# Optimization experiments

Measured on AMD Instinct MI355X. Metric: run time of the kernel, lower is better.

The kernel has to match this reference:

```python
import jax, jax.numpy as jnp
import numpy as np

EPS = 1e-6

def setup_inputs() -> dict:
    key = jax.random.key(0)
    ks = jax.random.split(key, 9)
    B, H, M = 8192, 1024, 16
    Hh = H // 2
    s = lambda k, shape, fan: jax.random.normal(k, shape, jnp.float32) * (1.0 / np.sqrt(fan))
    return {
        "query_embedding": jax.random.normal(ks[0], (B, H), jnp.float32),
        "cls1_w": s(ks[1], (Hh, H), H),
        "cls1_b": jnp.zeros((Hh,), jnp.float32),
        "cls3_w": s(ks[2], (M, Hh), Hh),
        "cls3_b": jnp.zeros((M,), jnp.float32),
        "exp_w1": s(ks[3], (M, Hh, H), H),
        "exp_b1": jnp.zeros((M, Hh), jnp.float32),
        "exp_w2": s(ks[4], (M, H, Hh), Hh),
        "exp_b2": jnp.zeros((M, H), jnp.float32),
    }

def _l2_normalize(x, eps=EPS):
    # F.normalize: x / clamp(||x||_2, min=eps)
    n = jnp.sqrt(jnp.sum(x * x, axis=-1, keepdims=True))
    return x / jnp.maximum(n, eps)

def reference(query_embedding, cls1_w, cls1_b, cls3_w, cls3_b,
              exp_w1, exp_b1, exp_w2, exp_b2):
    q = query_embedding  # [B, H]
    # --- cls(): gating network (eval, sbmoe_top1) ---
    x1 = jax.nn.relu(q @ cls1_w.T + cls1_b)          # [B, H/2]
    logits = x1 @ cls3_w.T + cls3_b                  # [B, M]
    probs = jax.nn.softmax(logits, axis=-1)          # [B, M]
    top1 = jnp.argmax(probs, axis=-1)                # [B]
    mask = jax.nn.one_hot(top1, probs.shape[-1], dtype=probs.dtype)
    gates = probs * mask                             # [B, M] (one nonzero/row)
    # --- query_embedder(): run all experts, gate, combine ---
    h = jax.nn.relu(jnp.einsum('bd,mhd->bmh', q, exp_w1) + exp_b1)   # [B, M, H/2]
    expert_out = jnp.einsum('bmh,mdh->bmd', h, exp_w2) + exp_b2      # [B, M, H]
    combined = jnp.einsum('bmd,bm->bd', expert_out, gates)           # [B, H]
    out = _l2_normalize(combined) + q
    return out
```

## Files before the change

### kernel.cpp

```cpp
#include <hip/hip_runtime.h>
#include <math.h>

#define NB 8192
#define H 1024
#define HH 512
#define NEXP 16
#define NT128 96
#define AMBIG_THR 1e-3f

typedef __attribute__((ext_vector_type(8))) short bfrag;
typedef __attribute__((ext_vector_type(4))) float f4;

__device__ __forceinline__ f4 MF(bfrag a, bfrag b, f4 c) {
    return __builtin_amdgcn_mfma_f32_16x16x32_bf16(a, b, c, 0, 0, 0);
}
__device__ __forceinline__ unsigned short f2bf(float f) {
    unsigned u = __float_as_uint(f);
    u += 0x7fff + ((u >> 16) & 1);
    return (unsigned short)(u >> 16);
}
__device__ __forceinline__ float bf2f(unsigned short h) {
    return __uint_as_float((unsigned)h << 16);
}

typedef __attribute__((address_space(1))) const unsigned GAS;
typedef __attribute__((address_space(3))) unsigned LAS;
__device__ __forceinline__ void gld16(const void* g, void* l) {
    __builtin_amdgcn_global_load_lds((GAS*)g, (LAS*)l, 16, 0, 0);
}

__global__ __launch_bounds__(256) void cvtA_kernel(
    const float* __restrict__ q, const float* __restrict__ w1, const float* __restrict__ w3,
    unsigned short* __restrict__ qhi, unsigned short* __restrict__ qlo,
    unsigned short* __restrict__ w1hi, unsigned short* __restrict__ w1lo,
    unsigned short* __restrict__ w3hi, unsigned short* __restrict__ w3lo,
    int* __restrict__ counts, int* __restrict__ ambig_cnt)
{
    const int b = blockIdx.x, t = threadIdx.x;
    if (b == 0) {
        if (t < NEXP) counts[t] = 0;
        if (t == NEXP) ambig_cnt[0] = 0;
    }
    const float* src; unsigned short *hi, *lo; int i;
    if (b < 8192)      { src = q;  hi = qhi;  lo = qlo;  i = b * 256 + t; }
    else if (b < 8704) { src = w1; hi = w1hi; lo = w1lo; i = (b - 8192) * 256 + t; }
    else               { src = w3; hi = w3hi; lo = w3lo; i = (b - 8704) * 256 + t; }
    float4 v = ((const float4*)src)[i];
    ushort4 h, l;
    h.x = f2bf(v.x); l.x = f2bf(v.x - bf2f(h.x));
    h.y = f2bf(v.y); l.y = f2bf(v.y - bf2f(h.y));
    h.z = f2bf(v.z); l.z = f2bf(v.z - bf2f(h.z));
    h.w = f2bf(v.w); l.w = f2bf(v.w - bf2f(h.w));
    ((ushort4*)hi)[i] = h;
    ((ushort4*)lo)[i] = l;
}

__global__ __launch_bounds__(256) void cvtB_kernel(
    const float* __restrict__ ew1, const float* __restrict__ ew2,
    unsigned short* __restrict__ d1, unsigned short* __restrict__ d2)
{
    const int b = blockIdx.x, t = threadIdx.x;
    const float* src; unsigned short* dst; int i;
    if (b < 8192) { src = ew1; dst = d1; i = b * 256 + t; }
    else          { src = ew2; dst = d2; i = (b - 8192) * 256 + t; }
    float4 v = ((const float4*)src)[i];
    ushort4 h;
    h.x = f2bf(v.x); h.y = f2bf(v.y); h.z = f2bf(v.z); h.w = f2bf(v.w);
    ((ushort4*)dst)[i] = h;
}

__global__ __launch_bounds__(256) void g1_kernel(
    const unsigned short* __restrict__ qhi, const unsigned short* __restrict__ qlo,
    const unsigned short* __restrict__ w1hi, const unsigned short* __restrict__ w1lo,
    const float* __restrict__ b1,
    unsigned short* __restrict__ x1hi, unsigned short* __restrict__ x1lo)
{
    __shared__ unsigned short Ah[3][128][32];
    __shared__ unsigned short Al[3][128][32];
    __shared__ unsigned short Bh[3][64][32];
    __shared__ unsigned short Bl[3][64][32];

    const int t = threadIdx.x, w = t >> 6, lane = t & 63;
    const int quad = lane >> 4, l16 = lane & 15;
    const int rowA0 = blockIdx.x * 128;
    const int colB0 = blockIdx.y * 64;
    const int rl = lane >> 2, sl = lane & 3;

    const unsigned short* gsrc[6];
    unsigned short* lbase[6];
    int bstr[6];
    #pragma unroll
    for (int j = 0; j < 6; ++j) {
        int c = w + j * 4;
        int rloc; const unsigned short* s; unsigned short* d; int str;
        if (c < 8)       { rloc = c * 16 + rl;        s = qhi  + (size_t)(rowA0 + rloc) * H; d = &Ah[0][c * 16][0];        str = 128 * 32; }
        else if (c < 16) { rloc = (c - 8) * 16 + rl;  s = qlo  + (size_t)(rowA0 + rloc) * H; d = &Al[0][(c - 8) * 16][0];  str = 128 * 32; }
        else if (c < 20) { rloc = (c - 16) * 16 + rl; s = w1hi + (size_t)(colB0 + rloc) * H; d = &Bh[0][(c - 16) * 16][0]; str = 64 * 32; }
        else             { rloc = (c - 20) * 16 + rl; s = w1lo + (size_t)(colB0 + rloc) * H; d = &Bl[0][(c - 20) * 16][0]; str = 64 * 32; }
        int f = (rloc & 3) ^ ((rloc >> 2) & 3);
        gsrc[j]  = s + (sl ^ f) * 8;
        lbase[j] = d;
        bstr[j]  = str;
    }

    const f4 z4 = {0.f, 0.f, 0.f, 0.f};
    f4 acc[2][4] = {{z4, z4, z4, z4}, {z4, z4, z4, z4}};
    const int sw = (quad ^ (l16 & 3) ^ (l16 >> 2)) * 8;
    const int ra0 = w * 32 + l16, ra1 = ra0 + 16;

    auto STAGE = [&](int buf, int kt) {
        #pragma unroll
        for (int j = 0; j < 6; ++j)
            gld16(gsrc[j] + kt * 32, lbase[j] + buf * bstr[j]);
    };
    auto COMPUTE = [&](int buf) {
        bfrag ah0 = *(const bfrag*)&Ah[buf][ra0][sw];
        bfrag al0 = *(const bfrag*)&Al[buf][ra0][sw];
        bfrag ah1 = *(const bfrag*)&Ah[buf][ra1][sw];
        bfrag al1 = *(const bfrag*)&Al[buf][ra1][sw];
        #pragma unroll
        for (int cb = 0; cb < 4; ++cb) {
            bfrag bh = *(const bfrag*)&Bh[buf][cb * 16 + l16][sw];
            bfrag bl = *(const bfrag*)&Bl[buf][cb * 16 + l16][sw];
            acc[0][cb] = MF(al0, bh, MF(ah0, bl, MF(ah0, bh, acc[0][cb])));
            acc[1][cb] = MF(al1, bh, MF(ah1, bl, MF(ah1, bh, acc[1][cb])));
        }
    };

    STAGE(0, 0);
    STAGE(1, 1);
    for (int kt = 0; kt < 32; ++kt) {
        if (kt < 31) asm volatile("s_waitcnt vmcnt(6)" ::: "memory");
        else         asm volatile("s_waitcnt vmcnt(0)" ::: "memory");
        __builtin_amdgcn_s_barrier();
        if (kt < 30) STAGE((kt + 2) % 3, kt + 2);
        COMPUTE(kt % 3);
    }

    const int row0 = rowA0 + w * 32;
    #pragma unroll
    for (int cb = 0; cb < 4; ++cb) {
        int col = colB0 + cb * 16 + l16;
        float bias = b1[col];
        #pragma unroll
        for (int rb = 0; rb < 2; ++rb)
            #pragma unroll
            for (int i = 0; i < 4; ++i) {
                int row = rb * 16 + quad * 4 + i;
                float v = fmaxf(acc[rb][cb][i] + bias, 0.f);
                unsigned short hh = f2bf(v);
                size_t idx = (size_t)(row0 + row) * HH + col;
                x1hi[idx] = hh;
                x1lo[idx] = f2bf(v - bf2f(hh));
            }
    }
}

__global__ __launch_bounds__(256) void logits_kernel(
    const unsigned short* __restrict__ x1hi, const unsigned short* __restrict__ x1lo,
    const unsigned short* __restrict__ w3hi, const unsigned short* __restrict__ w3lo,
    const float* __restrict__ b3,
    int* __restrict__ top1, float* __restrict__ gval, int* __restrict__ counts,
    int* __restrict__ ambig_rows, int* __restrict__ ambig_cnt)
{
    __shared__ float lgp[4][32][NEXP];
    const int t = threadIdx.x, wave = t >> 6, lane = t & 63;
    const int quad = lane >> 4, l16 = lane & 15;
    const int row0 = blockIdx.x * 32;
    const f4 z4 = {0.f, 0.f, 0.f, 0.f};

    f4 l0 = z4, l1 = z4;
    const size_t ar0 = (size_t)(row0 + l16) * HH + quad * 8;
    const size_t ar1 = ar0 + (size_t)16 * HH;
    const size_t br = (size_t)l16 * HH + quad * 8;
    #pragma unroll
    for (int ks = 0; ks < 4; ++ks) {
        int kk = wave * 128 + ks * 32;
        bfrag ah0 = *(const bfrag*)(x1hi + ar0 + kk);
        bfrag al0 = *(const bfrag*)(x1lo + ar0 + kk);
        bfrag ah1 = *(const bfrag*)(x1hi + ar1 + kk);
        bfrag al1 = *(const bfrag*)(x1lo + ar1 + kk);
        bfrag bh  = *(const bfrag*)(w3hi + br + kk);
        bfrag bl  = *(const bfrag*)(w3lo + br + kk);
        l0 = MF(al0, bh, MF(ah0, bl, MF(ah0, bh, l0)));
        l1 = MF(al1, bh, MF(ah1, bl, MF(ah1, bh, l1)));
    }
    #pragma unroll
    for (int i = 0; i < 4; ++i) {
        lgp[wave][quad * 4 + i][l16] = l0[i];
        lgp[wave][16 + quad * 4 + i][l16] = l1[i];
    }
    __syncthreads();

    if (t < 32) {
        float lg[NEXP];
        #pragma unroll
        for (int m = 0; m < NEXP; ++m)
            lg[m] = lgp[0][t][m] + lgp[1][t][m] + lgp[2][t][m] + lgp[3][t][m] + b3[m];
        float best = lg[0], second = -3.4e38f; int bi = 0;
        #pragma unroll
        for (int m = 1; m < NEXP; ++m) {
            float v = lg[m];
            if (v > best) { second = best; best = v; bi = m; }
            else if (v > second) second = v;
        }
        float se = 0.f;
        #pragma unroll
        for (int m = 0; m < NEXP; ++m) se += expf(lg[m] - best);
        int grow = row0 + t;
        top1[grow] = bi;
        gval[grow] = 1.f / se;
        atomicAdd(&counts[bi], 1);
        if (best - second < AMBIG_THR) {
            int pos = atomicAdd(ambig_cnt, 1);
            if (pos < NB) ambig_rows[pos] = grow;
        }
    }
}

__global__ __launch_bounds__(256) void fixup1_kernel(
    const float* __restrict__ q, const float* __restrict__ w1, const float* __restrict__ b1,
    const int* __restrict__ ambig_rows, const int* __restrict__ ambig_cnt,
    float* __restrict__ x1buf)
{
    __shared__ __align__(16) float qrow[H];
// ... 25 lines not shown
                s1 += __shfl_xor(s1, off, 64);
            }
            if (ln == 0) {
                x1buf[(size_t)ii * HH + c]     = fmaxf(s0 + b1[c], 0.f);
                x1buf[(size_t)ii * HH + c + 1] = fmaxf(s1 + b1[c + 1], 0.f);
            }
        }
        __syncthreads();
    }
}

__global__ __launch_bounds__(256) void fixup2_kernel(
    const float* __restrict__ x1buf,
    const float* __restrict__ w3, const float* __restrict__ b3,
    const int* __restrict__ ambig_rows, const int* __restrict__ ambig_cnt,
    int* __restrict__ top1, float* __restrict__ gval, int* __restrict__ counts)
{
    __shared__ float lgs[NEXP];
    const int t = threadIdx.x, wv = t >> 6, ln = t & 63;
    int nn = *ambig_cnt; if (nn > NB) nn = NB;
    for (int ii = blockIdx.x; ii < nn; ii += gridDim.x) {
        int row = ambig_rows[ii];
        const float4* xv = (const float4*)(x1buf + (size_t)ii * HH);
        for (int m = wv; m < NEXP; m += 4) {
            const float4* wr = (const float4*)(w3 + (size_t)m * HH);
            float s = 0.f;
            #pragma unroll
            for (int j = 0; j < 2; ++j) {
                float4 a = xv[j * 64 + ln];
                float4 b = wr[j * 64 + ln];
                s += a.x * b.x + a.y * b.y + a.z * b.z + a.w * b.w;
            }
            #pragma unroll
            for (int off = 32; off; off >>= 1) s += __shfl_xor(s, off, 64);
            if (ln == 0) lgs[m] = s + b3[m];
        }
        __syncthreads();
        if (t == 0) {
            float best = lgs[0]; int bi = 0;
            #pragma unroll
            for (int m = 1; m < NEXP; ++m) if (lgs[m] > best) { best = lgs[m]; bi = m; }
            float se = 0.f;
            #pragma unroll
            for (int m = 0; m < NEXP; ++m) se += expf(lgs[m] - best);
            int old = top1[row];
            if (bi != old) {
                atomicSub(&counts[old], 1);
                atomicAdd(&counts[bi], 1);
                top1[row] = bi;
            }
            gval[row] = 1.f / se;
        }
        __syncthreads();
    }
}

__global__ __launch_bounds__(256) void osc_kernel(
    const int* __restrict__ counts,
    int* __restrict__ tm_e, int* __restrict__ tm_p, int* __restrict__ tm_end,
    const int* __restrict__ top1, int* __restrict__ brows)
{
    __shared__ int sbpos[NEXP];
    const int t = threadIdx.x;
    if (t == 0) {
        int run = 0, tile = 0;
        for (int e = 0; e < NEXP; ++e) {
            sbpos[e] = run;
            int beg = run, end = run + counts[e];
            for (int p = beg; p < end; p += 128) {
                tm_e[tile] = e; tm_p[tile] = p; tm_end[tile] = end; ++tile;
            }
            run = end;
        }
        for (; tile < NT128; ++tile) tm_e[tile] = -1;
    }
    __syncthreads();
    for (int i = t; i < NB; i += 256) {
        int e = top1[i];
        int pos = atomicAdd(&sbpos[e], 1);
        brows[pos] = i;
    }
}

__global__ __launch_bounds__(256) void exp1_kernel(
    const unsigned short* __restrict__ qb, const unsigned short* __restrict__ ew1b,
    const float* __restrict__ eb1,
    const int* __restrict__ tm_e, const int* __restrict__ tm_p, const int* __restrict__ tm_end,
    const int* __restrict__ brows, unsigned short* __restrict__ h)
{
    const int e = tm_e[blockIdx.x];
    if (e < 0) return;
    const int p0 = tm_p[blockIdx.x], end = tm_end[blockIdx.x];

    __shared__ unsigned short A[3][128][32];
    __shared__ unsigned short B[3][64][32];

    const int t = threadIdx.x, w = t >> 6, lane = t & 63;
    const int quad = lane >> 4, l16 = lane & 15;
    const int c0 = blockIdx.y * 64;
    const unsigned short* w1p = ew1b + (size_t)e * HH * H;
    const int rl = lane >> 2, sl = lane & 3;

    const unsigned short* gsrc[3];
    unsigned short* lbase[3];
    int bstr[3];
    #pragma unroll
    for (int j = 0; j < 3; ++j) {
        int c = w + j * 4;
        int rloc; const unsigned short* s; unsigned short* d; int str;
        if (c < 8) {
            rloc = c * 16 + rl;
            int pa = p0 + rloc; if (pa >= end) pa = end - 1;
            s = qb + (size_t)brows[pa] * H;
            d = &A[0][c * 16][0]; str = 128 * 32;
        } else {
            rloc = (c - 8) * 16 + rl;
            s = w1p + (size_t)(c0 + rloc) * H;
            d = &B[0][(c - 8) * 16][0]; str = 64 * 32;
        }
        int f = (rloc & 3) ^ ((rloc >> 2) & 3);
        gsrc[j]  = s + (sl ^ f) * 8;
        lbase[j] = d;
        bstr[j]  = str;
    }

    const f4 z4 = {0.f, 0.f, 0.f, 0.f};
    f4 acc[2][4] = {{z4, z4, z4, z4}, {z4, z4, z4, z4}};
    const int sw = (quad ^ (l16 & 3) ^ (l16 >> 2)) * 8;
    const int ra0 = w * 32 + l16, ra1 = ra0 + 16;

    auto STAGE = [&](int buf, int kt) {
        #pragma unroll
        for (int j = 0; j < 3; ++j)
            gld16(gsrc[j] + kt * 32, lbase[j] + buf * bstr[j]);
    };
    auto COMPUTE = [&](int buf) {
        bfrag a0 = *(const bfrag*)&A[buf][ra0][sw];
        bfrag a1 = *(const bfrag*)&A[buf][ra1][sw];
        #pragma unroll
        for (int cb = 0; cb < 4; ++cb) {
            bfrag bb = *(const bfrag*)&B[buf][cb * 16 + l16][sw];
            acc[0][cb] = MF(a0, bb, acc[0][cb]);
            acc[1][cb] = MF(a1, bb, acc[1][cb]);
        }
    };

    STAGE(0, 0);
    STAGE(1, 1);
    for (int kt = 0; kt < 32; ++kt) {
        if (kt < 31) asm volatile("s_waitcnt vmcnt(3)" ::: "memory");
        else         asm volatile("s_waitcnt vmcnt(0)" ::: "memory");
        __builtin_amdgcn_s_barrier();
        if (kt < 30) STAGE((kt + 2) % 3, kt + 2);
        COMPUTE(kt % 3);
    }

    const int prow0 = p0 + w * 32;
    #pragma unroll
    for (int cb = 0; cb < 4; ++cb) {
        int col = c0 + cb * 16 + l16;
        float bias = eb1[e * HH + col];
        #pragma unroll
        for (int rb = 0; rb < 2; ++rb)
            #pragma unroll
            for (int i = 0; i < 4; ++i) {
                int row = rb * 16 + quad * 4 + i;
                if (prow0 + row < end)
                    h[(size_t)(prow0 + row) * HH + col] = f2bf(fmaxf(acc[rb][cb][i] + bias, 0.f));
            }
    }
}

__global__ __launch_bounds__(256) void exp2_kernel(
    const unsigned short* __restrict__ h, const unsigned short* __restrict__ ew2b,
    const float* __restrict__ eb2,
    const int* __restrict__ tm_e, const int* __restrict__ tm_p, const int* __restrict__ tm_end,
    const int* __restrict__ brows,
    float* __restrict__ vout, float* __restrict__ psum)
{
    const int e = tm_e[blockIdx.x];
    if (e < 0) return;
    const int p0 = tm_p[blockIdx.x], end = tm_end[blockIdx.x];

    __shared__ unsigned short A[3][128][32];
    __shared__ unsigned short B[3][64][32];

    const int t = threadIdx.x, w = t >> 6, lane = t & 63;
    const int quad = lane >> 4, l16 = lane & 15;
    const int cg = blockIdx.y;
    const int c0 = cg * 64;
    const unsigned short* w2p = ew2b + (size_t)e * H * HH;
    const int rl = lane >> 2, sl = lane & 3;

    const unsigned short* gsrc[3];
    unsigned short* lbase[3];
    int bstr[3];
    #pragma unroll
    for (int j = 0; j < 3; ++j) {
        int c = w + j * 4;
        int rloc; const unsigned short* s; unsigned short* d; int str;
        if (c < 8) {
            rloc = c * 16 + rl;
            int pa = p0 + rloc; if (pa >= end) pa = end - 1;
            s = h + (size_t)pa * HH;
            d = &A[0][c * 16][0]; str = 128 * 32;
        } else {
            rloc = (c - 8) * 16 + rl;
            s = w2p + (size_t)(c0 + rloc) * HH;
            d = &B[0][(c - 8) * 16][0]; str = 64 * 32;
        }
        int f = (rloc & 3) ^ ((rloc >> 2) & 3);
        gsrc[j]  = s + (sl ^ f) * 8;
        lbase[j] = d;
        bstr[j]  = str;
    }

    const f4 z4 = {0.f, 0.f, 0.f, 0.f};
    f4 acc[2][4] = {{z4, z4, z4, z4}, {z4, z4, z4, z4}};
    const int sw = (quad ^ (l16 & 3) ^ (l16 >> 2)) * 8;
    const int ra0 = w * 32 + l16, ra1 = ra0 + 16;

    auto STAGE = [&](int buf, int kt) {
        #pragma unroll
        for (int j = 0; j < 3; ++j)
            gld16(gsrc[j] + kt * 32, lbase[j] + buf * bstr[j]);
    };
    auto COMPUTE = [&](int buf) {
        bfrag a0 = *(const bfrag*)&A[buf][ra0][sw];
        bfrag a1 = *(const bfrag*)&A[buf][ra1][sw];
        #pragma unroll
        for (int cb = 0; cb < 4; ++cb) {
            bfrag bb = *(const bfrag*)&B[buf][cb * 16 + l16][sw];
            acc[0][cb] = MF(a0, bb, acc[0][cb]);
            acc[1][cb] = MF(a1, bb, acc[1][cb]);
        }
    };

    STAGE(0, 0);
    STAGE(1, 1);
    for (int kt = 0; kt < 16; ++kt) {
        if (kt < 15) asm volatile("s_waitcnt vmcnt(3)" ::: "memory");
        else         asm volatile("s_waitcnt vmcnt(0)" ::: "memory");
        __builtin_amdgcn_s_barrier();
        if (kt < 14) STAGE((kt + 2) % 3, kt + 2);
        COMPUTE(kt % 3);
    }

    const int pw0 = p0 + w * 32;
    float rs0[4] = {0.f, 0.f, 0.f, 0.f}, rs1[4] = {0.f, 0.f, 0.f, 0.f};
    #pragma unroll
    for (int i = 0; i < 4; ++i) {
        int row0i = quad * 4 + i, row1i = 16 + quad * 4 + i;
        int g0 = pw0 + row0i; if (g0 >= end) g0 = end - 1;
        int g1 = pw0 + row1i; if (g1 >= end) g1 = end - 1;
        int gr0 = brows[g0], gr1 = brows[g1];
        #pragma unroll
        for (int cb = 0; cb < 4; ++cb) {
            int col = c0 + cb * 16 + l16;
            float bias = eb2[e * H + col];
            float v0 = acc[0][cb][i] + bias;
            float v1 = acc[1][cb][i] + bias;
            vout[(size_t)gr0 * H + col] = v0;
            vout[(size_t)gr1 * H + col] = v1;
            rs0[i] += v0 * v0;
            rs1[i] += v1 * v1;
        }
    }
    #pragma unroll
    for (int i = 0; i < 4; ++i) {
        float s0 = rs0[i], s1 = rs1[i];
        #pragma unroll
        for (int off = 8; off; off >>= 1) {
            s0 += __shfl_xor(s0, off, 16);
            s1 += __shfl_xor(s1, off, 16);
        }
        if (l16 == 0) {
            int g0 = pw0 + quad * 4 + i;      if (g0 >= end) g0 = end - 1;
            int g1 = pw0 + 16 + quad * 4 + i; if (g1 >= end) g1 = end - 1;
            psum[(size_t)brows[g0] * 16 + cg] = s0;
            psum[(size_t)brows[g1] * 16 + cg] = s1;
        }
    }
}

__global__ __launch_bounds__(256) void finalize_kernel(
    float* __restrict__ out, const float* __restrict__ q,
    const float* __restrict__ psum, const float* __restrict__ gval)
{
    const int row = blockIdx.x, t = threadIdx.x;
    float s = 0.f;
    #pragma unroll
    for (int j = 0; j < 16; ++j) s += psum[(size_t)row * 16 + j];
    float g = gval[row];
    float sc = g / fmaxf(g * sqrtf(s), 1e-6f);
    size_t i = (size_t)row * 256 + t;
    float4 v = ((const float4*)out)[i];
    float4 qq = ((const float4*)q)[i];
    float4 o;
    o.x = v.x * sc + qq.x;
    o.y = v.y * sc + qq.y;
    o.z = v.z * sc + qq.z;
    o.w = v.w * sc + qq.w;
    ((float4*)out)[i] = o;
}

extern "C" void kernel_launch(void* const* d_in, const int* in_sizes, int n_in,
                              void* d_out, int out_size, void* d_ws, size_t ws_size,
                              hipStream_t stream) {
    const float* q      = (const float*)d_in[0];
    const float* cls1_w = (const float*)d_in[1];
    const float* cls1_b = (const float*)d_in[2];
    const float* cls3_w = (const float*)d_in[3];
    const float* cls3_b = (const float*)d_in[4];
    const float* exp_w1 = (const float*)d_in[5];
    const float* exp_b1 = (const float*)d_in[6];
    const float* exp_w2 = (const float*)d_in[7];
    const float* exp_b2 = (const float*)d_in[8];
    float* out = (float*)d_out;

    char* w = (char*)d_ws;
    float* psum   = (float*)w;              w += (size_t)NB * 16 * 4;
    float* gvalp  = (float*)w;              w += (size_t)NB * 4;
    int* top1     = (int*)w;                w += (size_t)NB * 4;
    int* brows    = (int*)w;                w += (size_t)NB * 4;
    int* ambig_rows = (int*)w;              w += (size_t)NB * 4;
    int* counts   = (int*)w;                w += 16 * 4;
    int* offsets  = (int*)w;                w += 16 * 4;
    int* bpos     = (int*)w;                w += 16 * 4;
    int* ambig_cnt = (int*)w;               w += 4 * 4;
    int* tm_e     = (int*)w;                w += NT128 * 4;
    int* tm_p     = (int*)w;                w += NT128 * 4;
    int* tm_end   = (int*)w;                w += NT128 * 4;
    w = (char*)(((size_t)w + 15) & ~(size_t)15);
    unsigned short* qhi  = (unsigned short*)w;  w += (size_t)NB * H * 2;
    unsigned short* qlo  = (unsigned short*)w;  w += (size_t)NB * H * 2;
    unsigned short* x1hi = (unsigned short*)w;
    unsigned short* x1lo = x1hi + (size_t)NB * HH;  w += (size_t)NB * HH * 2 * 2;
    unsigned short* hbuf = (unsigned short*)w;  w += (size_t)NB * HH * 2;
    unsigned short* w1hi = (unsigned short*)w;  w += (size_t)HH * H * 2;
    unsigned short* w1lo = (unsigned short*)w;  w += (size_t)HH * H * 2;
    unsigned short* w3hi = (unsigned short*)w;  w += (size_t)NEXP * HH * 2;
    unsigned short* w3lo = (unsigned short*)w;  w += (size_t)NEXP * HH * 2;
    unsigned short* ew1b = x1hi;
    unsigned short* ew2b = qlo;
    float* x1buf = (float*)x1hi;
    (void)offsets; (void)bpos;

    cvtA_kernel<<<8712, 256, 0, stream>>>(q, cls1_w, cls3_w, qhi, qlo, w1hi, w1lo,
                                          w3hi, w3lo, counts, ambig_cnt);
    g1_kernel<<<dim3(NB / 128, 8), 256, 0, stream>>>(qhi, qlo, w1hi, w1lo, cls1_b, x1hi, x1lo);
    logits_kernel<<<NB / 32, 256, 0, stream>>>(x1hi, x1lo, w3hi, w3lo, cls3_b,
                                               top1, gvalp, counts, ambig_rows, ambig_cnt);
    fixup1_kernel<<<256, 256, 0, stream>>>(q, cls1_w, cls1_b, ambig_rows, ambig_cnt, x1buf);
    fixup2_kernel<<<64, 256, 0, stream>>>(x1buf, cls3_w, cls3_b, ambig_rows, ambig_cnt,
                                          top1, gvalp, counts);
    cvtB_kernel<<<16384, 256, 0, stream>>>(exp_w1, exp_w2, ew1b, ew2b);
    osc_kernel<<<1, 256, 0, stream>>>(counts, tm_e, tm_p, tm_end, top1, brows);
    exp1_kernel<<<dim3(NT128, 8), 256, 0, stream>>>(qhi, ew1b, exp_b1,
                                                    tm_e, tm_p, tm_end, brows, hbuf);
    exp2_kernel<<<dim3(NT128, 16), 256, 0, stream>>>(hbuf, ew2b, exp_b2,
                                                     tm_e, tm_p, tm_end, brows, out, psum);
    finalize_kernel<<<NB, 256, 0, stream>>>(out, q, psum, gvalp);
}
```

Measured before the change: 356.6 us.

## Fuse fp32-to-bf16 conversion of query and expert weights into GEMM tile loads

Removes the standalone conversion passes over the query and the expert weights. The GEMM kernels now stage raw fp32 tiles into LDS with a swizzled layout and split them into bf16 hi/lo (or hi only) in registers just before the MFMA. This drops several large global read/write round trips (about 64MB of query conversion plus the expert weight conversion) and one launch. In exchange it doubles LDS footprint and staging traffic per tile, adds conversion ALU work inside the inner loop, and re-reads fp32 weights in every tile that uses them.

```diff
diff --git a/kernel.cpp b/kernel.cpp
--- a/kernel.cpp
+++ b/kernel.cpp
@@ -22,6 +22,24 @@
 __device__ __forceinline__ float bf2f(unsigned short h) {
     return __uint_as_float((unsigned)h << 16);
 }
+__device__ __forceinline__ void cvt_split8(const float* f, bfrag& hi, bfrag& lo) {
+    #pragma unroll
+    for (int i = 0; i < 8; ++i) {
+        unsigned short h = f2bf(f[i]);
+        hi[i] = (short)h;
+        lo[i] = (short)f2bf(f[i] - bf2f(h));
+    }
+}
+__device__ __forceinline__ bfrag cvt_hi8(const float* f) {
+    bfrag r;
+    #pragma unroll
+    for (int i = 0; i < 8; ++i) r[i] = (short)f2bf(f[i]);
+    return r;
+}
+__device__ __forceinline__ void ldf8(const char* rowbase, int f, int quad, float* out) {
+    *(float4*)&out[0] = *(const float4*)(rowbase + (((2 * quad)     ^ f) << 4));
+    *(float4*)&out[4] = *(const float4*)(rowbase + (((2 * quad + 1) ^ f) << 4));
+}
 
 typedef __attribute__((address_space(1))) const unsigned GAS;
 typedef __attribute__((address_space(3))) unsigned LAS;
@@ -29,9 +47,8 @@
     __builtin_amdgcn_global_load_lds((GAS*)g, (LAS*)l, 16, 0, 0);
 }
 
-__global__ __launch_bounds__(256) void cvtA_kernel(
-    const float* __restrict__ q, const float* __restrict__ w1, const float* __restrict__ w3,
-    unsigned short* __restrict__ qhi, unsigned short* __restrict__ qlo,
+__global__ __launch_bounds__(256) void cvtW_kernel(
+    const float* __restrict__ w1, const float* __restrict__ w3,
     unsigned short* __restrict__ w1hi, unsigned short* __restrict__ w1lo,
     unsigned short* __restrict__ w3hi, unsigned short* __restrict__ w3lo,
     int* __restrict__ counts, int* __restrict__ ambig_cnt)
@@ -42,9 +59,8 @@
         if (t == NEXP) ambig_cnt[0] = 0;
     }
     const float* src; unsigned short *hi, *lo; int i;
-    if (b < 8192)      { src = q;  hi = qhi;  lo = qlo;  i = b * 256 + t; }
-    else if (b < 8704) { src = w1; hi = w1hi; lo = w1lo; i = (b - 8192) * 256 + t; }
-    else               { src = w3; hi = w3hi; lo = w3lo; i = (b - 8704) * 256 + t; }
+    if (b < 512) { src = w1; hi = w1hi; lo = w1lo; i = b * 256 + t; }
+    else         { src = w3; hi = w3hi; lo = w3lo; i = (b - 512) * 256 + t; }
     float4 v = ((const float4*)src)[i];
     ushort4 h, l;
     h.x = f2bf(v.x); l.x = f2bf(v.x - bf2f(h.x));
@@ -55,28 +71,13 @@
     ((ushort4*)lo)[i] = l;
 }
 
-__global__ __launch_bounds__(256) void cvtB_kernel(
-    const float* __restrict__ ew1, const float* __restrict__ ew2,
-    unsigned short* __restrict__ d1, unsigned short* __restrict__ d2)
-{
-    const int b = blockIdx.x, t = threadIdx.x;
-    const float* src; unsigned short* dst; int i;
-    if (b < 8192) { src = ew1; dst = d1; i = b * 256 + t; }
-    else          { src = ew2; dst = d2; i = (b - 8192) * 256 + t; }
-    float4 v = ((const float4*)src)[i];
-    ushort4 h;
-    h.x = f2bf(v.x); h.y = f2bf(v.y); h.z = f2bf(v.z); h.w = f2bf(v.w);
-    ((ushort4*)dst)[i] = h;
-}
-
 __global__ __launch_bounds__(256) void g1_kernel(
-    const unsigned short* __restrict__ qhi, const unsigned short* __restrict__ qlo,
+    const float* __restrict__ qf,
     const unsigned short* __restrict__ w1hi, const unsigned short* __restrict__ w1lo,
     const float* __restrict__ b1,
     unsigned short* __restrict__ x1hi, unsigned short* __restrict__ x1lo)
 {
-    __shared__ unsigned short Ah[3][128][32];
-    __shared__ unsigned short Al[3][128][32];
+    __shared__ float          Aq[3][128][32];
     __shared__ unsigned short Bh[3][64][32];
     __shared__ unsigned short Bl[3][64][32];
 
@@ -84,40 +85,48 @@
     const int quad = lane >> 4, l16 = lane & 15;
     const int rowA0 = blockIdx.x * 128;
     const int colB0 = blockIdx.y * 64;
-    const int rl = lane >> 2, sl = lane & 3;
-
-    const unsigned short* gsrc[6];
-    unsigned short* lbase[6];
-    int bstr[6];
+
+    const char* gsrc[6]; char* lbase[6]; int bstr[6], kst[6];
     #pragma unroll
     for (int j = 0; j < 6; ++j) {
         int c = w + j * 4;
-        int rloc; const unsigned short* s; unsigned short* d; int str;
-        if (c < 8)       { rloc = c * 16 + rl;        s = qhi  + (size_t)(rowA0 + rloc) * H; d = &Ah[0][c * 16][0];        str = 128 * 32; }
-        else if (c < 16) { rloc = (c - 8) * 16 + rl;  s = qlo  + (size_t)(rowA0 + rloc) * H; d = &Al[0][(c - 8) * 16][0];  str = 128 * 32; }
-        else if (c < 20) { rloc = (c - 16) * 16 + rl; s = w1hi + (size_t)(colB0 + rloc) * H; d = &Bh[0][(c - 16) * 16][0]; str = 64 * 32; }
-        else             { rloc = (c - 20) * 16 + rl; s = w1lo + (size_t)(colB0 + rloc) * H; d = &Bl[0][(c - 20) * 16][0]; str = 64 * 32; }
-        int f = (rloc & 3) ^ ((rloc >> 2) & 3);
-        gsrc[j]  = s + (sl ^ f) * 8;
-        lbase[j] = d;
-        bstr[j]  = str;
+        if (c < 16) {
+            int rl = lane >> 3, sl = lane & 7;
+            int row = c * 8 + rl;
+            gsrc[j] = (const char*)(qf + (size_t)(rowA0 + row) * H + ((sl ^ (row & 7)) << 2));
+            lbase[j] = (char*)&Aq[0][c * 8][0];
+            bstr[j] = 128 * 32 * 4; kst[j] = 32 * 4;
+        } else {
+            int rl = lane >> 2, sl = lane & 3;
+            int row = ((c - 16) & 3) * 16 + rl;
+            int f = (row & 3) ^ ((row >> 2) & 3);
+            const unsigned short* s = (c < 20) ? w1hi : w1lo;
+            gsrc[j] = (const char*)(s + (size_t)(colB0 + row) * H + ((sl ^ f) << 3));
+            lbase[j] = (c < 20) ? (char*)&Bh[0][row - rl + rl][0] : (char*)&Bl[0][row - rl + rl][0];
+            lbase[j] = (c < 20) ? (char*)&Bh[0][((c - 16) & 3) * 16][0]
+                                : (char*)&Bl[0][((c - 16) & 3) * 16][0];
+            bstr[j] = 64 * 32 * 2; kst[j] = 32 * 2;
+        }
     }
 
     const f4 z4 = {0.f, 0.f, 0.f, 0.f};
     f4 acc[2][4] = {{z4, z4, z4, z4}, {z4, z4, z4, z4}};
     const int sw = (quad ^ (l16 & 3) ^ (l16 >> 2)) * 8;
+    const int fa = l16 & 7;
     const int ra0 = w * 32 + l16, ra1 = ra0 + 16;
 
     auto STAGE = [&](int buf, int kt) {
         #pragma unroll
         for (int j = 0; j < 6; ++j)
-            gld16(gsrc[j] + kt * 32, lbase[j] + buf * bstr[j]);
+            gld16(gsrc[j] + (size_t)kt * kst[j], lbase[j] + (size_t)buf * bstr[j]);
     };
     auto COMPUTE = [&](int buf) {
-        bfrag ah0 = *(const bfrag*)&Ah[buf][ra0][sw];
-        bfrag al0 = *(const bfrag*)&Al[buf][ra0][sw];
-        bfrag ah1 = *(const bfrag*)&Ah[buf][ra1][sw];
-        bfrag al1 = *(const bfrag*)&Al[buf][ra1][sw];
+        float fa0[8], fa1[8];
+        ldf8((const char*)&Aq[buf][ra0][0], fa, quad, fa0);
+        ldf8((const char*)&Aq[buf][ra1][0], fa, quad, fa1);
+        bfrag ah0, al0, ah1, al1;
+        cvt_split8(fa0, ah0, al0);
+        cvt_split8(fa1, ah1, al1);
         #pragma unroll
         for (int cb = 0; cb < 4; ++cb) {
             bfrag bh = *(const bfrag*)&Bh[buf][cb * 16 + l16][sw];
@@ -333,7 +342,7 @@
 }
 
 __global__ __launch_bounds__(256) void exp1_kernel(
-    const unsigned short* __restrict__ qb, const unsigned short* __restrict__ ew1b,
+    const float* __restrict__ qf, const float* __restrict__ ew1,
     const float* __restrict__ eb1,
     const int* __restrict__ tm_e, const int* __restrict__ tm_p, const int* __restrict__ tm_end,
     const int* __restrict__ brows, unsigned short* __restrict__ h)
@@ -342,54 +351,53 @@
     if (e < 0) return;
     const int p0 = tm_p[blockIdx.x], end = tm_end[blockIdx.x];
 
-    __shared__ unsigned short A[3][128][32];
-    __shared__ unsigned short B[3][64][32];
+    __shared__ float Aq[3][128][32];
+    __shared__ float Bw[3][64][32];
 
     const int t = threadIdx.x, w = t >> 6, lane = t & 63;
     const int quad = lane >> 4, l16 = lane & 15;
     const int c0 = blockIdx.y * 64;
-    const unsigned short* w1p = ew1b + (size_t)e * HH * H;
-    const int rl = lane >> 2, sl = lane & 3;
-
-    const unsigned short* gsrc[3];
-    unsigned short* lbase[3];
-    int bstr[3];
-    #pragma unroll
-    for (int j = 0; j < 3; ++j) {
+    const float* w1p = ew1 + (size_t)e * HH * H;
+    const int rl = lane >> 3, sl = lane & 7;
+
+    const char* gsrc[6]; char* lbase[6]; int bstr[6];
+    #pragma unroll
+    for (int j = 0; j < 6; ++j) {
         int c = w + j * 4;
-        int rloc; const unsigned short* s; unsigned short* d; int str;
-        if (c < 8) {
-            rloc = c * 16 + rl;
-            int pa = p0 + rloc; if (pa >= end) pa = end - 1;
-            s = qb + (size_t)brows[pa] * H;
-            d = &A[0][c * 16][0]; str = 128 * 32;
+        if (c < 16) {
+            int row = c * 8 + rl;
+            int pa = p0 + row; if (pa >= end) pa = end - 1;
+            gsrc[j] = (const char*)(qf + (size_t)brows[pa] * H + ((sl ^ (row & 7)) << 2));
+            lbase[j] = (char*)&Aq[0][c * 8][0];
+            bstr[j] = 128 * 32 * 4;
         } else {
-            rloc = (c - 8) * 16 + rl;
-            s = w1p + (size_t)(c0 + rloc) * H;
-            d = &B[0][(c - 8) * 16][0]; str = 64 * 32;
-        }
-        int f = (rloc & 3) ^ ((rloc >> 2) & 3);
-        gsrc[j]  = s + (sl ^ f) * 8;
-        lbase[j] = d;
-        bstr[j]  = str;
+            int row = (c - 16) * 8 + rl;
+            gsrc[j] = (const char*)(w1p + (size_t)(c0 + row) * H + ((sl ^ (row & 7)) << 2));
+            lbase[j] = (char*)&Bw[0][(c - 16) * 8][0];
+            bstr[j] = 64 * 32 * 4;
+        }
     }
 
     const f4 z4 = {0.f, 0.f, 0.f, 0.f};
     f4 acc[2][4] = {{z4, z4, z4, z4}, {z4, z4, z4, z4}};
-    const int sw = (quad ^ (l16 & 3) ^ (l16 >> 2)) * 8;
+    const int fa = l16 & 7;
     const int ra0 = w * 32 + l16, ra1 = ra0 + 16;
 
     auto STAGE = [&](int buf, int kt) {
         #pragma unroll
-        for (int j = 0; j < 3; ++j)
-            gld16(gsrc[j] + kt * 32, lbase[j] + buf * bstr[j]);
+        for (int j = 0; j < 6; ++j)
+            gld16(gsrc[j] + (size_t)kt * 128, lbase[j] + (size_t)buf * bstr[j]);
     };
     auto COMPUTE = [&](int buf) {
-        bfrag a0 = *(const bfrag*)&A[buf][ra0][sw];
-        bfrag a1 = *(const bfrag*)&A[buf][ra1][sw];
+        float f0[8], f1[8];
+        ldf8((const char*)&Aq[buf][ra0][0], fa, quad, f0);
+        ldf8((const char*)&Aq[buf][ra1][0], fa, quad, f1);
+        bfrag a0 = cvt_hi8(f0), a1 = cvt_hi8(f1);
         #pragma unroll
         for (int cb = 0; cb < 4; ++cb) {
-            bfrag bb = *(const bfrag*)&B[buf][cb * 16 + l16][sw];
+            float fb[8];
+            ldf8((const char*)&Bw[buf][cb * 16 + l16][0], fa, quad, fb);
+            bfrag bb = cvt_hi8(fb);
             acc[0][cb] = MF(a0, bb, acc[0][cb]);
             acc[1][cb] = MF(a1, bb, acc[1][cb]);
         }
@@ -398,7 +406,7 @@
     STAGE(0, 0);
     STAGE(1, 1);
     for (int kt = 0; kt < 32; ++kt) {
-        if (kt < 31) asm volatile("s_waitcnt vmcnt(3)" ::: "memory");
+        if (kt < 31) asm volatile("s_waitcnt vmcnt(6)" ::: "memory");
         else         asm volatile("s_waitcnt vmcnt(0)" ::: "memory");
         __builtin_amdgcn_s_barrier();
         if (kt < 30) STAGE((kt + 2) % 3, kt + 2);
@@ -422,7 +430,7 @@
 }
 
 __global__ __launch_bounds__(256) void exp2_kernel(
-    const unsigned short* __restrict__ h, const unsigned short* __restrict__ ew2b,
+    const unsigned short* __restrict__ h, const float* __restrict__ ew2,
     const float* __restrict__ eb2,
     const int* __restrict__ tm_e, const int* __restrict__ tm_p, const int* __restrict__ tm_end,
     const int* __restrict__ brows,
@@ -432,55 +440,55 @@
     if (e < 0) return;
     const int p0 = tm_p[blockIdx.x], end = tm_end[blockIdx.x];
 
-    __shared__ unsigned short A[3][128][32];
-    __shared__ unsigned short B[3][64][32];
+    __shared__ unsigned short Ah[3][128][32];
+    __shared__ float          Bw[3][64][32];
 
     const int t = threadIdx.x, w = t >> 6, lane = t & 63;
     const int quad = lane >> 4, l16 = lane & 15;
     const int cg = blockIdx.y;
     const int c0 = cg * 64;
-    const unsigned short* w2p = ew2b + (size_t)e * H * HH;
-    const int rl = lane >> 2, sl = lane & 3;
-
-    const unsigned short* gsrc[3];
-    unsigned short* lbase[3];
-    int bstr[3];
-    #pragma unroll
-    for (int j = 0; j < 3; ++j) {
+    const float* w2p = ew2 + (size_t)e * H * HH;
+
+    const char* gsrc[4]; char* lbase[4]; int bstr[4], kst[4];
+    #pragma unroll
+    for (int j = 0; j < 4; ++j) {
         int c = w + j * 4;
-        int rloc; const unsigned short* s; unsigned short* d; int str;
         if (c < 8) {
-            rloc = c * 16 + rl;
-            int pa = p0 + rloc; if (pa >= end) pa = end - 1;
-            s = h + (size_t)pa * HH;
-            d = &A[0][c * 16][0]; str = 128 * 32;
+            int rl = lane >> 2, sl = lane & 3;
+            int row = c * 16 + rl;
+            int pa = p0 + row; if (pa >= end) pa = end - 1;
+            int f = (row & 3) ^ ((row >> 2) & 3);
+            gsrc[j] = (const char*)(h + (size_t)pa * HH + ((sl ^ f) << 3));
+            lbase[j] = (char*)&Ah[0][c * 16][0];
+            bstr[j] = 128 * 32 * 2; kst[j] = 32 * 2;
         } else {
-            rloc = (c - 8) * 16 + rl;
-            s = w2p + (size_t)(c0 + rloc) * HH;
-            d = &B[0][(c - 8) * 16][0]; str = 64 * 32;
-        }
-        int f = (rloc & 3) ^ ((rloc >> 2) & 3);
-        gsrc[j]  = s + (sl ^ f) * 8;
-        lbase[j] = d;
-        bstr[j]  = str;
+            int rl = lane >> 3, sl = lane & 7;
+            int row = (c - 8) * 8 + rl;
+            gsrc[j] = (const char*)(w2p + (size_t)(c0 + row) * HH + ((sl ^ (row & 7)) << 2));
+            lbase[j] = (char*)&Bw[0][(c - 8) * 8][0];
+            bstr[j] = 64 * 32 * 4; kst[j] = 32 * 4;
+        }
     }
 
     const f4 z4 = {0.f, 0.f, 0.f, 0.f};
     f4 acc[2][4] = {{z4, z4, z4, z4}, {z4, z4, z4, z4}};
     const int sw = (quad ^ (l16 & 3) ^ (l16 >> 2)) * 8;
+    const int fa = l16 & 7;
     const int ra0 = w * 32 + l16, ra1 = ra0 + 16;
 
     auto STAGE = [&](int buf, int kt) {
         #pragma unroll
-        for (int j = 0; j < 3; ++j)
-            gld16(gsrc[j] + kt * 32, lbase[j] + buf * bstr[j]);
+        for (int j = 0; j < 4; ++j)
+            gld16(gsrc[j] + (size_t)kt * kst[j], lbase[j] + (size_t)buf * bstr[j]);
     };
     auto COMPUTE = [&](int buf) {
-        bfrag a0 = *(const bfrag*)&A[buf][ra0][sw];
-        bfrag a1 = *(const bfrag*)&A[buf][ra1][sw];
+        bfrag a0 = *(const bfrag*)&Ah[buf][ra0][sw];
+        bfrag a1 = *(const bfrag*)&Ah[buf][ra1][sw];
         #pragma unroll
         for (int cb = 0; cb < 4; ++cb) {
-            bfrag bb = *(const bfrag*)&B[buf][cb * 16 + l16][sw];
+            float fb[8];
+            ldf8((const char*)&Bw[buf][cb * 16 + l16][0], fa, quad, fb);
+            bfrag bb = cvt_hi8(fb);
             acc[0][cb] = MF(a0, bb, acc[0][cb]);
             acc[1][cb] = MF(a1, bb, acc[1][cb]);
         }
@@ -489,7 +497,7 @@
     STAGE(0, 0);
     STAGE(1, 1);
     for (int kt = 0; kt < 16; ++kt) {
-        if (kt < 15) asm volatile("s_waitcnt vmcnt(3)" ::: "memory");
+        if (kt < 15) asm volatile("s_waitcnt vmcnt(4)" ::: "memory");
         else         asm volatile("s_waitcnt vmcnt(0)" ::: "memory");
         __builtin_amdgcn_s_barrier();
         if (kt < 14) STAGE((kt + 2) % 3, kt + 2);
@@ -575,15 +583,11 @@
     int* brows    = (int*)w;                w += (size_t)NB * 4;
     int* ambig_rows = (int*)w;              w += (size_t)NB * 4;
     int* counts   = (int*)w;                w += 16 * 4;
-    int* offsets  = (int*)w;                w += 16 * 4;
-    int* bpos     = (int*)w;                w += 16 * 4;
     int* ambig_cnt = (int*)w;               w += 4 * 4;
     int* tm_e     = (int*)w;                w += NT128 * 4;
     int* tm_p     = (int*)w;                w += NT128 * 4;
     int* tm_end   = (int*)w;                w += NT128 * 4;
     w = (char*)(((size_t)w + 15) & ~(size_t)15);
-    unsigned short* qhi  = (unsigned short*)w;  w += (size_t)NB * H * 2;
-    unsigned short* qlo  = (unsigned short*)w;  w += (size_t)NB * H * 2;
     unsigned short* x1hi = (unsigned short*)w;
     unsigned short* x1lo = x1hi + (size_t)NB * HH;  w += (size_t)NB * HH * 2 * 2;
     unsigned short* hbuf = (unsigned short*)w;  w += (size_t)NB * HH * 2;
@@ -591,24 +595,20 @@
     unsigned short* w1lo = (unsigned short*)w;  w += (size_t)HH * H * 2;
     unsigned short* w3hi = (unsigned short*)w;  w += (size_t)NEXP * HH * 2;
     unsigned short* w3lo = (unsigned short*)w;  w += (size_t)NEXP * HH * 2;
-    unsigned short* ew1b = x1hi;
-    unsigned short* ew2b = qlo;
     float* x1buf = (float*)x1hi;
-    (void)offsets; (void)bpos;
-
-    cvtA_kernel<<<8712, 256, 0, stream>>>(q, cls1_w, cls3_w, qhi, qlo, w1hi, w1lo,
-                                          w3hi, w3lo, counts, ambig_cnt);
-    g1_kernel<<<dim3(NB / 128, 8), 256, 0, stream>>>(qhi, qlo, w1hi, w1lo, cls1_b, x1hi, x1lo);
+
+    cvtW_kernel<<<520, 256, 0, stream>>>(cls1_w, cls3_w, w1hi, w1lo, w3hi, w3lo,
+                                         counts, ambig_cnt);
+    g1_kernel<<<dim3(NB / 128, 8), 256, 0, stream>>>(q, w1hi, w1lo, cls1_b, x1hi, x1lo);
     logits_kernel<<<NB / 32, 256, 0, stream>>>(x1hi, x1lo, w3hi, w3lo, cls3_b,
                                                top1, gvalp, counts, ambig_rows, ambig_cnt);
     fixup1_kernel<<<256, 256, 0, stream>>>(q, cls1_w, cls1_b, ambig_rows, ambig_cnt, x1buf);
     fixup2_kernel<<<64, 256, 0, stream>>>(x1buf, cls3_w, cls3_b, ambig_rows, ambig_cnt,
                                           top1, gvalp, counts);
-    cvtB_kernel<<<16384, 256, 0, stream>>>(exp_w1, exp_w2, ew1b, ew2b);
     osc_kernel<<<1, 256, 0, stream>>>(counts, tm_e, tm_p, tm_end, top1, brows);
-    exp1_kernel<<<dim3(NT128, 8), 256, 0, stream>>>(qhi, ew1b, exp_b1,
+    exp1_kernel<<<dim3(NT128, 8), 256, 0, stream>>>(q, exp_w1, exp_b1,
                                                     tm_e, tm_p, tm_end, brows, hbuf);
-    exp2_kernel<<<dim3(NT128, 16), 256, 0, stream>>>(hbuf, ew2b, exp_b2,
+    exp2_kernel<<<dim3(NT128, 16), 256, 0, stream>>>(hbuf, exp_w2, exp_b2,
                                                      tm_e, tm_p, tm_end, brows, out, psum);
     finalize_kernel<<<NB, 256, 0, stream>>>(out, q, psum, gvalp);
 }
```

Result: slower. 425.4 us (+19.3%).

## Widen GEMM block tiles to 128x128 with 8 waves in g1, exp1, exp2

Applied to the files above, without the earlier changes.

The three main GEMM kernels now use 512-thread blocks covering a 128x128 output tile instead of 256 threads on 128x64, with waves arranged as a 4x2 grid. Each A tile loaded into shared memory is reused across twice as many columns, which cuts global and LDS traffic per output. The cost is double the shared memory per block and half as many blocks, which lowers occupancy and grid parallelism, especially in the expert kernels that have few tiles. The psum slot index and the vmcnt wait counts are updated to match the new layout.

```diff
diff --git a/kernel.cpp b/kernel.cpp
--- a/kernel.cpp
+++ b/kernel.cpp
@@ -69,7 +69,7 @@
     ((ushort4*)dst)[i] = h;
 }
 
-__global__ __launch_bounds__(256) void g1_kernel(
+__global__ __launch_bounds__(512) void g1_kernel(
     const unsigned short* __restrict__ qhi, const unsigned short* __restrict__ qlo,
     const unsigned short* __restrict__ w1hi, const unsigned short* __restrict__ w1lo,
     const float* __restrict__ b1,
@@ -77,41 +77,42 @@
 {
     __shared__ unsigned short Ah[3][128][32];
     __shared__ unsigned short Al[3][128][32];
-    __shared__ unsigned short Bh[3][64][32];
-    __shared__ unsigned short Bl[3][64][32];
+    __shared__ unsigned short Bh[3][128][32];
+    __shared__ unsigned short Bl[3][128][32];
 
     const int t = threadIdx.x, w = t >> 6, lane = t & 63;
     const int quad = lane >> 4, l16 = lane & 15;
+    const int wr = w & 3, wc = w >> 2;
     const int rowA0 = blockIdx.x * 128;
-    const int colB0 = blockIdx.y * 64;
+    const int colB0 = blockIdx.y * 128;
     const int rl = lane >> 2, sl = lane & 3;
 
-    const unsigned short* gsrc[6];
-    unsigned short* lbase[6];
-    int bstr[6];
-    #pragma unroll
-    for (int j = 0; j < 6; ++j) {
-        int c = w + j * 4;
-        int rloc; const unsigned short* s; unsigned short* d; int str;
-        if (c < 8)       { rloc = c * 16 + rl;        s = qhi  + (size_t)(rowA0 + rloc) * H; d = &Ah[0][c * 16][0];        str = 128 * 32; }
-        else if (c < 16) { rloc = (c - 8) * 16 + rl;  s = qlo  + (size_t)(rowA0 + rloc) * H; d = &Al[0][(c - 8) * 16][0];  str = 128 * 32; }
-        else if (c < 20) { rloc = (c - 16) * 16 + rl; s = w1hi + (size_t)(colB0 + rloc) * H; d = &Bh[0][(c - 16) * 16][0]; str = 64 * 32; }
-        else             { rloc = (c - 20) * 16 + rl; s = w1lo + (size_t)(colB0 + rloc) * H; d = &Bl[0][(c - 20) * 16][0]; str = 64 * 32; }
+    const unsigned short* gsrc[4];
+    unsigned short* lbase[4];
+    #pragma unroll
+    for (int j = 0; j < 4; ++j) {
+        int c = w + j * 8;
+        int rloc; const unsigned short* s; unsigned short* d;
+        if (c < 8)       { rloc = c * 16 + rl;        s = qhi  + (size_t)(rowA0 + rloc) * H; d = &Ah[0][c * 16][0]; }
+        else if (c < 16) { rloc = (c - 8) * 16 + rl;  s = qlo  + (size_t)(rowA0 + rloc) * H; d = &Al[0][(c - 8) * 16][0]; }
+        else if (c < 24) { rloc = (c - 16) * 16 + rl; s = w1hi + (size_t)(colB0 + rloc) * H; d = &Bh[0][(c - 16) * 16][0]; }
+        else             { rloc = (c - 24) * 16 + rl; s = w1lo + (size_t)(colB0 + rloc) * H; d = &Bl[0][(c - 24) * 16][0]; }
         int f = (rloc & 3) ^ ((rloc >> 2) & 3);
         gsrc[j]  = s + (sl ^ f) * 8;
         lbase[j] = d;
-        bstr[j]  = str;
-    }
+    }
+    const int bstr = 128 * 32;
 
     const f4 z4 = {0.f, 0.f, 0.f, 0.f};
     f4 acc[2][4] = {{z4, z4, z4, z4}, {z4, z4, z4, z4}};
     const int sw = (quad ^ (l16 & 3) ^ (l16 >> 2)) * 8;
-    const int ra0 = w * 32 + l16, ra1 = ra0 + 16;
+    const int ra0 = wr * 32 + l16, ra1 = ra0 + 16;
+    const int cbase = wc * 64;
 
     auto STAGE = [&](int buf, int kt) {
         #pragma unroll
-        for (int j = 0; j < 6; ++j)
-            gld16(gsrc[j] + kt * 32, lbase[j] + buf * bstr[j]);
+        for (int j = 0; j < 4; ++j)
+            gld16(gsrc[j] + kt * 32, lbase[j] + buf * bstr);
     };
     auto COMPUTE = [&](int buf) {
         bfrag ah0 = *(const bfrag*)&Ah[buf][ra0][sw];
@@ -120,8 +121,8 @@
         bfrag al1 = *(const bfrag*)&Al[buf][ra1][sw];
         #pragma unroll
         for (int cb = 0; cb < 4; ++cb) {
-            bfrag bh = *(const bfrag*)&Bh[buf][cb * 16 + l16][sw];
-            bfrag bl = *(const bfrag*)&Bl[buf][cb * 16 + l16][sw];
+            bfrag bh = *(const bfrag*)&Bh[buf][cbase + cb * 16 + l16][sw];
+            bfrag bl = *(const bfrag*)&Bl[buf][cbase + cb * 16 + l16][sw];
             acc[0][cb] = MF(al0, bh, MF(ah0, bl, MF(ah0, bh, acc[0][cb])));
             acc[1][cb] = MF(al1, bh, MF(ah1, bl, MF(ah1, bh, acc[1][cb])));
         }
@@ -130,17 +131,17 @@
     STAGE(0, 0);
     STAGE(1, 1);
     for (int kt = 0; kt < 32; ++kt) {
-        if (kt < 31) asm volatile("s_waitcnt vmcnt(6)" ::: "memory");
+        if (kt < 31) asm volatile("s_waitcnt vmcnt(4)" ::: "memory");
         else         asm volatile("s_waitcnt vmcnt(0)" ::: "memory");
         __builtin_amdgcn_s_barrier();
         if (kt < 30) STAGE((kt + 2) % 3, kt + 2);
         COMPUTE(kt % 3);
     }
 
-    const int row0 = rowA0 + w * 32;
+    const int row0 = rowA0 + wr * 32;
     #pragma unroll
     for (int cb = 0; cb < 4; ++cb) {
-        int col = colB0 + cb * 16 + l16;
+        int col = colB0 + cbase + cb * 16 + l16;
         float bias = b1[col];
         #pragma unroll
         for (int rb = 0; rb < 2; ++rb)
@@ -332,7 +333,7 @@
     }
 }
 
-__global__ __launch_bounds__(256) void exp1_kernel(
+__global__ __launch_bounds__(512) void exp1_kernel(
     const unsigned short* __restrict__ qb, const unsigned short* __restrict__ ew1b,
     const float* __restrict__ eb1,
     const int* __restrict__ tm_e, const int* __restrict__ tm_p, const int* __restrict__ tm_end,
@@ -343,53 +344,54 @@
     const int p0 = tm_p[blockIdx.x], end = tm_end[blockIdx.x];
 
     __shared__ unsigned short A[3][128][32];
-    __shared__ unsigned short B[3][64][32];
+    __shared__ unsigned short B[3][128][32];
 
     const int t = threadIdx.x, w = t >> 6, lane = t & 63;
     const int quad = lane >> 4, l16 = lane & 15;
-    const int c0 = blockIdx.y * 64;
+    const int wr = w & 3, wc = w >> 2;
+    const int c0 = blockIdx.y * 128;
     const unsigned short* w1p = ew1b + (size_t)e * HH * H;
     const int rl = lane >> 2, sl = lane & 3;
 
-    const unsigned short* gsrc[3];
-    unsigned short* lbase[3];
-    int bstr[3];
-    #pragma unroll
-    for (int j = 0; j < 3; ++j) {
-        int c = w + j * 4;
-        int rloc; const unsigned short* s; unsigned short* d; int str;
+    const unsigned short* gsrc[2];
+    unsigned short* lbase[2];
+    #pragma unroll
+    for (int j = 0; j < 2; ++j) {
+        int c = w + j * 8;
+        int rloc; const unsigned short* s; unsigned short* d;
         if (c < 8) {
             rloc = c * 16 + rl;
             int pa = p0 + rloc; if (pa >= end) pa = end - 1;
             s = qb + (size_t)brows[pa] * H;
-            d = &A[0][c * 16][0]; str = 128 * 32;
+            d = &A[0][c * 16][0];
         } else {
             rloc = (c - 8) * 16 + rl;
             s = w1p + (size_t)(c0 + rloc) * H;
-            d = &B[0][(c - 8) * 16][0]; str = 64 * 32;
+            d = &B[0][(c - 8) * 16][0];
         }
         int f = (rloc & 3) ^ ((rloc >> 2) & 3);
         gsrc[j]  = s + (sl ^ f) * 8;
         lbase[j] = d;
-        bstr[j]  = str;
-    }
+    }
+    const int bstr = 128 * 32;
 
     const f4 z4 = {0.f, 0.f, 0.f, 0.f};
     f4 acc[2][4] = {{z4, z4, z4, z4}, {z4, z4, z4, z4}};
     const int sw = (quad ^ (l16 & 3) ^ (l16 >> 2)) * 8;
-    const int ra0 = w * 32 + l16, ra1 = ra0 + 16;
+    const int ra0 = wr * 32 + l16, ra1 = ra0 + 16;
+    const int cbase = wc * 64;
 
     auto STAGE = [&](int buf, int kt) {
         #pragma unroll
-        for (int j = 0; j < 3; ++j)
-            gld16(gsrc[j] + kt * 32, lbase[j] + buf * bstr[j]);
+        for (int j = 0; j < 2; ++j)
+            gld16(gsrc[j] + kt * 32, lbase[j] + buf * bstr);
     };
     auto COMPUTE = [&](int buf) {
         bfrag a0 = *(const bfrag*)&A[buf][ra0][sw];
         bfrag a1 = *(const bfrag*)&A[buf][ra1][sw];
         #pragma unroll
         for (int cb = 0; cb < 4; ++cb) {
-            bfrag bb = *(const bfrag*)&B[buf][cb * 16 + l16][sw];
+            bfrag bb = *(const bfrag*)&B[buf][cbase + cb * 16 + l16][sw];
             acc[0][cb] = MF(a0, bb, acc[0][cb]);
             acc[1][cb] = MF(a1, bb, acc[1][cb]);
         }
@@ -398,17 +400,17 @@
     STAGE(0, 0);
     STAGE(1, 1);
     for (int kt = 0; kt < 32; ++kt) {
-        if (kt < 31) asm volatile("s_waitcnt vmcnt(3)" ::: "memory");
+        if (kt < 31) asm volatile("s_waitcnt vmcnt(2)" ::: "memory");
         else         asm volatile("s_waitcnt vmcnt(0)" ::: "memory");
         __builtin_amdgcn_s_barrier();
         if (kt < 30) STAGE((kt + 2) % 3, kt + 2);
         COMPUTE(kt % 3);
     }
 
-    const int prow0 = p0 + w * 32;
+    const int prow0 = p0 + wr * 32;
     #pragma unroll
     for (int cb = 0; cb < 4; ++cb) {
-        int col = c0 + cb * 16 + l16;
+        int col = c0 + cbase + cb * 16 + l16;
         float bias = eb1[e * HH + col];
         #pragma unroll
         for (int rb = 0; rb < 2; ++rb)
@@ -421,7 +423,7 @@
     }
 }
 
-__global__ __launch_bounds__(256) void exp2_kernel(
+__global__ __launch_bounds__(512) void exp2_kernel(
     const unsigned short* __restrict__ h, const unsigned short* __restrict__ ew2b,
     const float* __restrict__ eb2,
     const int* __restrict__ tm_e, const int* __restrict__ tm_p, const int* __restrict__ tm_end,
@@ -433,54 +435,54 @@
     const int p0 = tm_p[blockIdx.x], end = tm_end[blockIdx.x];
 
     __shared__ unsigned short A[3][128][32];
-    __shared__ unsigned short B[3][64][32];
+    __shared__ unsigned short B[3][128][32];
 
     const int t = threadIdx.x, w = t >> 6, lane = t & 63;
     const int quad = lane >> 4, l16 = lane & 15;
-    const int cg = blockIdx.y;
-    const int c0 = cg * 64;
+    const int wr = w & 3, wc = w >> 2;
+    const int c0 = blockIdx.y * 128;
     const unsigned short* w2p = ew2b + (size_t)e * H * HH;
     const int rl = lane >> 2, sl = lane & 3;
 
-    const unsigned short* gsrc[3];
-    unsigned short* lbase[3];
-    int bstr[3];
-    #pragma unroll
-    for (int j = 0; j < 3; ++j) {
-        int c = w + j * 4;
-        int rloc; const unsigned short* s; unsigned short* d; int str;
+    const unsigned short* gsrc[2];
+    unsigned short* lbase[2];
+    #pragma unroll
+    for (int j = 0; j < 2; ++j) {
+        int c = w + j * 8;
+        int rloc; const unsigned short* s; unsigned short* d;
         if (c < 8) {
             rloc = c * 16 + rl;
             int pa = p0 + rloc; if (pa >= end) pa = end - 1;
             s = h + (size_t)pa * HH;
-            d = &A[0][c * 16][0]; str = 128 * 32;
+            d = &A[0][c * 16][0];
         } else {
             rloc = (c - 8) * 16 + rl;
             s = w2p + (size_t)(c0 + rloc) * HH;
-            d = &B[0][(c - 8) * 16][0]; str = 64 * 32;
+            d = &B[0][(c - 8) * 16][0];
         }
         int f = (rloc & 3) ^ ((rloc >> 2) & 3);
         gsrc[j]  = s + (sl ^ f) * 8;
         lbase[j] = d;
-        bstr[j]  = str;
-    }
+    }
+    const int bstr = 128 * 32;
 
     const f4 z4 = {0.f, 0.f, 0.f, 0.f};
     f4 acc[2][4] = {{z4, z4, z4, z4}, {z4, z4, z4, z4}};
     const int sw = (quad ^ (l16 & 3) ^ (l16 >> 2)) * 8;
-    const int ra0 = w * 32 + l16, ra1 = ra0 + 16;
+    const int ra0 = wr * 32 + l16, ra1 = ra0 + 16;
+    const int cbase = wc * 64;
 
     auto STAGE = [&](int buf, int kt) {
         #pragma unroll
-        for (int j = 0; j < 3; ++j)
-            gld16(gsrc[j] + kt * 32, lbase[j] + buf * bstr[j]);
+        for (int j = 0; j < 2; ++j)
+            gld16(gsrc[j] + kt * 32, lbase[j] + buf * bstr);
     };
     auto COMPUTE = [&](int buf) {
         bfrag a0 = *(const bfrag*)&A[buf][ra0][sw];
         bfrag a1 = *(const bfrag*)&A[buf][ra1][sw];
         #pragma unroll
         for (int cb = 0; cb < 4; ++cb) {
-            bfrag bb = *(const bfrag*)&B[buf][cb * 16 + l16][sw];
+            bfrag bb = *(const bfrag*)&B[buf][cbase + cb * 16 + l16][sw];
             acc[0][cb] = MF(a0, bb, acc[0][cb]);
             acc[1][cb] = MF(a1, bb, acc[1][cb]);
         }
@@ -489,14 +491,15 @@
     STAGE(0, 0);
     STAGE(1, 1);
     for (int kt = 0; kt < 16; ++kt) {
-        if (kt < 15) asm volatile("s_waitcnt vmcnt(3)" ::: "memory");
+        if (kt < 15) asm volatile("s_waitcnt vmcnt(2)" ::: "memory");
         else         asm volatile("s_waitcnt vmcnt(0)" ::: "memory");
         __builtin_amdgcn_s_barrier();
         if (kt < 14) STAGE((kt + 2) % 3, kt + 2);
         COMPUTE(kt % 3);
     }
 
-    const int pw0 = p0 + w * 32;
+    const int pw0 = p0 + wr * 32;
+    const int slot = blockIdx.y * 2 + wc;
     float rs0[4] = {0.f, 0.f, 0.f, 0.f}, rs1[4] = {0.f, 0.f, 0.f, 0.f};
     #pragma unroll
     for (int i = 0; i < 4; ++i) {
@@ -506,7 +509,7 @@
         int gr0 = brows[g0], gr1 = brows[g1];
         #pragma unroll
         for (int cb = 0; cb < 4; ++cb) {
-            int col = c0 + cb * 16 + l16;
+            int col = c0 + cbase + cb * 16 + l16;
             float bias = eb2[e * H + col];
             float v0 = acc[0][cb][i] + bias;
             float v1 = acc[1][cb][i] + bias;
@@ -527,8 +530,8 @@
         if (l16 == 0) {
             int g0 = pw0 + quad * 4 + i;      if (g0 >= end) g0 = end - 1;
             int g1 = pw0 + 16 + quad * 4 + i; if (g1 >= end) g1 = end - 1;
-            psum[(size_t)brows[g0] * 16 + cg] = s0;
-            psum[(size_t)brows[g1] * 16 + cg] = s1;
+            psum[(size_t)brows[g0] * 16 + slot] = s0;
+            psum[(size_t)brows[g1] * 16 + slot] = s1;
         }
     }
 }
@@ -575,8 +578,6 @@
     int* brows    = (int*)w;                w += (size_t)NB * 4;
     int* ambig_rows = (int*)w;              w += (size_t)NB * 4;
     int* counts   = (int*)w;                w += 16 * 4;
-    int* offsets  = (int*)w;                w += 16 * 4;
-    int* bpos     = (int*)w;                w += 16 * 4;
     int* ambig_cnt = (int*)w;               w += 4 * 4;
     int* tm_e     = (int*)w;                w += NT128 * 4;
     int* tm_p     = (int*)w;                w += NT128 * 4;
@@ -594,11 +595,10 @@
     unsigned short* ew1b = x1hi;
     unsigned short* ew2b = qlo;
     float* x1buf = (float*)x1hi;
-    (void)offsets; (void)bpos;
 
     cvtA_kernel<<<8712, 256, 0, stream>>>(q, cls1_w, cls3_w, qhi, qlo, w1hi, w1lo,
                                           w3hi, w3lo, counts, ambig_cnt);
-    g1_kernel<<<dim3(NB / 128, 8), 256, 0, stream>>>(qhi, qlo, w1hi, w1lo, cls1_b, x1hi, x1lo);
+    g1_kernel<<<dim3(NB / 128, 4), 512, 0, stream>>>(qhi, qlo, w1hi, w1lo, cls1_b, x1hi, x1lo);
     logits_kernel<<<NB / 32, 256, 0, stream>>>(x1hi, x1lo, w3hi, w3lo, cls3_b,
                                                top1, gvalp, counts, ambig_rows, ambig_cnt);
     fixup1_kernel<<<256, 256, 0, stream>>>(q, cls1_w, cls1_b, ambig_rows, ambig_cnt, x1buf);
@@ -606,9 +606,9 @@
                                           top1, gvalp, counts);
     cvtB_kernel<<<16384, 256, 0, stream>>>(exp_w1, exp_w2, ew1b, ew2b);
     osc_kernel<<<1, 256, 0, stream>>>(counts, tm_e, tm_p, tm_end, top1, brows);
-    exp1_kernel<<<dim3(NT128, 8), 256, 0, stream>>>(qhi, ew1b, exp_b1,
+    exp1_kernel<<<dim3(NT128, 4), 512, 0, stream>>>(qhi, ew1b, exp_b1,
                                                     tm_e, tm_p, tm_end, brows, hbuf);
-    exp2_kernel<<<dim3(NT128, 16), 256, 0, stream>>>(hbuf, ew2b, exp_b2,
-                                                     tm_e, tm_p, tm_end, brows, out, psum);
+    exp2_kernel<<<dim3(NT128, 8), 512, 0, stream>>>(hbuf, ew2b, exp_b2,
+                                                    tm_e, tm_p, tm_end, brows, out, psum);
     finalize_kernel<<<NB, 256, 0, stream>>>(out, q, psum, gvalp);
 }
```

New measurement: 359.0 us. About the same (+0.7%).
